# Optimization experiments

Measured on AMD Instinct MI355X. Metric: run time of the kernel, lower is better.

Reference implementation:

```python
import jax, jax.numpy as jnp
import numpy as np

EMBED_DIM = 1024
NUM_HEADS = 16
HEAD_DIM = EMBED_DIM // NUM_HEADS
KERNEL = 3
PAD = KERNEL // 2
B, L = 4, 1024


def conv1d(x, w, b):
    # x: [B, D, L], w: [D_out, D_in, K], b: [D_out]; 'same' padding like nn.Conv1d(padding=K//2)
    y = jax.lax.conv_general_dilated(
        x, w, window_strides=(1,), padding=[(PAD, PAD)],
        dimension_numbers=('NCH', 'OIH', 'NCH'))
    return y + b[None, :, None]


def setup_inputs() -> dict:
    key = jax.random.key(0)
    ks = jax.random.split(key, 12)
    fan = EMBED_DIM * KERNEL
    bound = 1.0 / np.sqrt(fan)
    def wconv(k):
        return jax.random.uniform(k, (EMBED_DIM, EMBED_DIM, KERNEL), jnp.float32, -bound, bound)
    def bconv(k):
        return jax.random.uniform(k, (EMBED_DIM,), jnp.float32, -bound, bound)
    return {
        'query': jax.random.normal(ks[0], (B, L, EMBED_DIM), jnp.float32),
        'key': jax.random.normal(ks[1], (B, L, EMBED_DIM), jnp.float32),
        'value': jax.random.normal(ks[2], (B, L, EMBED_DIM), jnp.float32),
        'key_padding_mask': jax.random.randint(ks[3], (B, L), 0, 2) > 0,
        'attn_mask': jnp.zeros((L, L), jnp.float32),
        'q_w': wconv(ks[4]), 'q_b': bconv(ks[5]),
        'k_w': wconv(ks[6]), 'k_b': bconv(ks[7]),
        'v_w': wconv(ks[8]), 'v_b': bconv(ks[9]),
        'o_w': wconv(ks[10]), 'o_b': bconv(ks[11]),
    }


def reference(query, key, value, key_padding_mask, attn_mask,
              q_w, q_b, k_w, k_b, v_w, v_b, o_w, o_b):
    scale = HEAD_DIM ** -0.5
    # projections: [B, D, L]
    q = conv1d(jnp.swapaxes(query, 1, 2), q_w, q_b)
    k = conv1d(jnp.swapaxes(key, 1, 2), k_w, k_b)
    v = conv1d(jnp.swapaxes(value, 1, 2), v_w, v_b)
    # [B, H, d, L]
    q = q.reshape(B, NUM_HEADS, HEAD_DIM, L)
    k = k.reshape(B, NUM_HEADS, HEAD_DIM, L)
    v = v.reshape(B, NUM_HEADS, HEAD_DIM, L)
    # scores: [B, H, L, L]
    scores = jnp.einsum('bhdi,bhdj->bhij', q, k) * scale
    scores = scores + attn_mask[None, None, :, :]
    scores = jnp.where(key_padding_mask[:, None, None, :], -jnp.inf, scores)
    attn = jax.nn.softmax(scores, axis=-1)  # dropout p=0 (eval) -> identity
    out = jnp.einsum('bhij,bhdj->bhdi', attn, v)  # [B, H, d, L]
    out = out.reshape(B, EMBED_DIM, L)
    out = conv1d(out, o_w, o_b)
    return jnp.swapaxes(out, 1, 2)  # [B, L, D]
```

## Files before the change

kernel.cpp:

```cpp
#include <hip/hip_runtime.h>
#include <math.h>

#define NB 4
#define NL 1024
#define ND 1024
#define NH 16
#define HD 64

typedef __attribute__((ext_vector_type(8))) short bf16x8;
typedef __attribute__((ext_vector_type(4))) float f32x4;

static __device__ __forceinline__ unsigned short f32_to_bf16(float f) {
  unsigned u = __float_as_uint(f);
  u += 0x7FFFu + ((u >> 16) & 1u);
  return (unsigned short)(u >> 16);
}
static __device__ __forceinline__ float bf16_to_f32(unsigned short s) {
  return __uint_as_float(((unsigned)s) << 16);
}

static __device__ __forceinline__ void split8(float4 a, float4 b, bf16x8* hi, bf16x8* lo) {
  unsigned u[8] = {__float_as_uint(a.x), __float_as_uint(a.y),
                   __float_as_uint(a.z), __float_as_uint(a.w),
                   __float_as_uint(b.x), __float_as_uint(b.y),
                   __float_as_uint(b.z), __float_as_uint(b.w)};
  union { unsigned p[4]; bf16x8 v; } H, L;
#pragma unroll
  for (int p = 0; p < 4; ++p) {
    unsigned u0 = u[2 * p], u1 = u[2 * p + 1];
    H.p[p] = __builtin_amdgcn_perm(u1, u0, 0x07060302u);
    unsigned l0 = __float_as_uint(__uint_as_float(u0) - __uint_as_float(u0 & 0xFFFF0000u));
    unsigned l1 = __float_as_uint(__uint_as_float(u1) - __uint_as_float(u1 & 0xFFFF0000u));
    L.p[p] = __builtin_amdgcn_perm(l1, l0, 0x07060302u);
  }
  *hi = H.v; *lo = L.v;
}

__global__ __launch_bounds__(256) void wcvt_kernel(
    const float* __restrict__ w0, const float* __restrict__ w1,
    const float* __restrict__ w2, const float* __restrict__ w3,
    unsigned short* __restrict__ wb, int* __restrict__ flag)
{
  if (blockIdx.x == 0 && blockIdx.y == 0 && threadIdx.x == 0) flag[0] = 0;
  const int t = blockIdx.y;
  const int o = blockIdx.x;
  const float* w = (t == 0) ? w0 : (t == 1) ? w1 : (t == 2) ? w2 : w3;
  unsigned short* hi = wb + (size_t)t * 6 * (1u << 20);
  unsigned short* lo = hi + 3 * (1u << 20);
  const int tid = threadIdx.x;
  float v[12];
  const float* src = w + (size_t)o * (ND * 3) + tid * 12;
#pragma unroll
  for (int j = 0; j < 3; ++j) {
    float4 f = *(const float4*)(src + j * 4);
    v[j * 4 + 0] = f.x; v[j * 4 + 1] = f.y; v[j * 4 + 2] = f.z; v[j * 4 + 3] = f.w;
  }
#pragma unroll
  for (int k = 0; k < 3; ++k) {
    unsigned short hh[4], ll[4];
#pragma unroll
    for (int ii = 0; ii < 4; ++ii) {
      float x = v[ii * 3 + k];
      unsigned short h = f32_to_bf16(x);
      float r = x - bf16_to_f32(h);
      hh[ii] = h; ll[ii] = f32_to_bf16(r);
    }
    size_t dst = (size_t)k * (ND * ND) + (size_t)o * ND + tid * 4;
    *(ushort4*)&hi[dst] = make_ushort4(hh[0], hh[1], hh[2], hh[3]);
    *(ushort4*)&lo[dst] = make_ushort4(ll[0], ll[1], ll[2], ll[3]);
  }
}

__global__ __launch_bounds__(256) void amask_scan(
    const float* __restrict__ a, int* __restrict__ flag)
{
  size_t i = ((size_t)blockIdx.x * 256 + threadIdx.x) * 4;
  float4 v = *(const float4*)&a[i];
  if (v.x != 0.f || v.y != 0.f || v.z != 0.f || v.w != 0.f) atomicOr(flag, 1);
}

__global__ __launch_bounds__(256, 3) void conv_mfma2(
    const float* X0, const float* X1, const float* X2,
    const unsigned short* __restrict__ wb,
    const float* b0, const float* b1, const float* b2,
    float* Y0, float* Y1, float* Y2, int mode)
{
  __shared__ float Af[128 * 32];
  __shared__ unsigned short Bh[128 * 32];
  __shared__ unsigned short Bl[128 * 32];

  const int tid = threadIdx.x, lane = tid & 63, wave = tid >> 6;
  const int lin = blockIdx.x + 8 * (blockIdx.y + 32 * blockIdx.z);
  const int g = lin & 7, t = lin >> 3;
  const int nb = (g & 3) * 2 + (t & 1);
  const int mb = (g >> 2) * 16 + ((t >> 1) & 15);
  const int z  = t >> 5;
  const int n0 = nb * 128, m0 = mb * 128;
  const int b = m0 >> 10, l0v = m0 & (NL - 1);

  const float* X = (mode == 0) ? (z == 0 ? X0 : (z == 1 ? X1 : X2)) : X0;
  const unsigned short* Wh = (mode == 0) ? wb + (size_t)z * 6 * (1u << 20) : wb;
  const unsigned short* Wl = Wh + 3 * (1u << 20);

  const int wm = (wave >> 1) * 64, wn = (wave & 1) * 64;
  const int mrow = lane & 15, quad = lane >> 4;
  const int r16 = lane >> 2, cs = lane & 3;
  const int src_chunk = (cs - (r16 >> 1)) & 3;
  const int bswz = ((quad + (mrow >> 1)) & 3) * 8;

  f32x4 acc[4][4] = {};

  const int kbeg = (mode == 0) ? 0 : z;
  const int kend = (mode == 0) ? 3 : z + 1;
  for (int koff = kbeg; koff < kend; ++koff) {
    const bool edge_lo = (l0v == 0 && koff == 0);
    const bool edge_hi = (l0v == NL - 128 && koff == 2);
    for (int i0 = 0; i0 < ND; i0 += 32) {
#pragma unroll
      for (int s = 0; s < 2; ++s) {
        const int seg = wave * 2 + s;
        const size_t goff = ((size_t)koff << 20) +
                            (size_t)(n0 + seg * 16 + r16) * ND + i0 + src_chunk * 8;
        __builtin_amdgcn_global_load_lds(
            (const __attribute__((address_space(1))) unsigned int*)(Wh + goff),
            (__attribute__((address_space(3))) unsigned int*)&Bh[seg * 512], 16, 0, 0);
        __builtin_amdgcn_global_load_lds(
            (const __attribute__((address_space(1))) unsigned int*)(Wl + goff),
            (__attribute__((address_space(3))) unsigned int*)&Bl[seg * 512], 16, 0, 0);
      }
#pragma unroll
      for (int j = 0; j < 4; ++j) {
        const int s = (wave * 4 + j) * 64 + lane;
        const int row = s >> 3, sir = s & 7;
        const int chunk = (sir - (row & 7)) & 7;
        int l = l0v + row + koff - 1;
        l = (l < 0) ? 0 : (l > NL - 1 ? NL - 1 : l);
        const float* gp = X + ((size_t)(b << 10) + l) * ND + i0 + chunk * 4;
        __builtin_amdgcn_global_load_lds(
            (const __attribute__((address_space(1))) unsigned int*)gp,
            (__attribute__((address_space(3))) unsigned int*)&Af[(wave * 4 + j) * 256],
            16, 0, 0);
      }
      __syncthreads();
      if (edge_lo || edge_hi) {
        const int er = edge_lo ? 0 : 127;
        if (tid < 8) *(float4*)&Af[er * 32 + tid * 4] = make_float4(0.f, 0.f, 0.f, 0.f);
        __syncthreads();
      }
      bf16x8 ah[4], al[4];
#pragma unroll
      for (int mi = 0; mi < 4; ++mi) {
        const int row = wm + mi * 16 + mrow, r7 = row & 7;
        float4 fa = *(const float4*)&Af[row * 32 + (((quad * 2) + r7) & 7) * 4];
        float4 fb = *(const float4*)&Af[row * 32 + (((quad * 2 + 1) + r7) & 7) * 4];
        split8(fa, fb, &ah[mi], &al[mi]);
      }
#pragma unroll
      for (int ni = 0; ni < 4; ++ni) {
        const int brow = wn + ni * 16 + mrow;
        bf16x8 bh = *(const bf16x8*)&Bh[brow * 32 + bswz];
        bf16x8 bl = *(const bf16x8*)&Bl[brow * 32 + bswz];
#pragma unroll
        for (int mi = 0; mi < 4; ++mi) {
          acc[mi][ni] = __builtin_amdgcn_mfma_f32_16x16x32_bf16(ah[mi], bh, acc[mi][ni], 0, 0, 0);
          acc[mi][ni] = __builtin_amdgcn_mfma_f32_16x16x32_bf16(ah[mi], bl, acc[mi][ni], 0, 0, 0);
          acc[mi][ni] = __builtin_amdgcn_mfma_f32_16x16x32_bf16(al[mi], bh, acc[mi][ni], 0, 0, 0);
        }
      }
      __syncthreads();
    }
  }

  if (mode == 0) {
    float* Y = (z == 0) ? Y0 : (z == 1 ? Y1 : Y2);
    const float* bias = (z == 0) ? b0 : (z == 1 ? b1 : b2);
#pragma unroll
    for (int ni = 0; ni < 4; ++ni) {
      const int n = n0 + wn + ni * 16 + mrow;
      const float bv = bias[n];
      const int h = n >> 6, dd = n & 63;
#pragma unroll
      for (int mi = 0; mi < 4; ++mi) {
        const int mbase = m0 + wm + mi * 16 + quad * 4;
        f32x4 v = acc[mi][ni];
#pragma unroll
        for (int r = 0; r < 4; ++r) {
          const int l = (mbase + r) & (NL - 1);
          Y[(((size_t)b * NH + h) * NL + l) * HD + dd] = v[r] + bv;
        }
      }
    }
  } else {
    float* P = Y0 + (size_t)z * ((size_t)NB * NL * ND);
#pragma unroll
    for (int ni = 0; ni < 4; ++ni) {
      const int n = n0 + wn + ni * 16 + mrow;
#pragma unroll
      for (int mi = 0; mi < 4; ++mi) {
        const int mbase = m0 + wm + mi * 16 + quad * 4;
        f32x4 v = acc[mi][ni];
#pragma unroll
        for (int r = 0; r < 4; ++r) {
          const int l = (mbase + r) & (NL - 1);
          P[((size_t)(b << 10) + l) * ND + n] = v[r];
        }
      }
    }
  }
}

__global__ __launch_bounds__(256) void reduce_kernel(
    const float* __restrict__ P, const float* __restrict__ bias, float* __restrict__ out)
{
  const size_t S = (size_t)NB * NL * ND;
  const size_t idx = ((size_t)blockIdx.x * 256 + threadIdx.x) * 4;
  const int n = (int)(idx & (ND - 1));
  float4 p0 = *(const float4*)&P[idx];
  float4 p1 = *(const float4*)&P[idx + S];
  float4 p2 = *(const float4*)&P[idx + 2 * S];
  float4 bv = *(const float4*)&bias[n];
  float4 r;
  r.x = p0.x + p1.x + p2.x + bv.x;
  r.y = p0.y + p1.y + p2.y + bv.y;
  r.z = p0.z + p1.z + p2.z + bv.z;
  r.w = p0.w + p1.w + p2.w + bv.w;
  *(float4*)&out[idx] = r;
}

__global__ __launch_bounds__(256, 3) void attn_mfma(
    const float* __restrict__ qT, const float* __restrict__ kT,
    const float* __restrict__ vT, const int* __restrict__ kpm,
    const float* __restrict__ amask, const int* __restrict__ aflagp,
    float* __restrict__ AO)
{
  __shared__ __align__(16) unsigned short S[3 * 64 * 72];
  unsigned short* Kh = S;
  unsigned short* Kl = S + 4608;
  unsigned short* Vt = S + 2 * 4608;

  const int tid = threadIdx.x, lane = tid & 63, wave = tid >> 6;
  const int c = lane & 15, quad = lane >> 4;
  const int lin = blockIdx.x;
  const int bh = (lin & 7) + 8 * (lin >> 7);
  const int mt = (lin >> 3) & 15;
  const int b = bh >> 4;
  const int m0 = mt * 64;
  const size_t base = (size_t)bh * NL * HD;
  const int aflag = *aflagp;
  const int mrow = wave * 16 + c;
  const int gm = m0 + mrow;

  const int sr = tid >> 2, scq = tid & 3;

#pragma unroll
  for (int ii = 0; ii < 2; ++ii) {
    const int c8 = scq * 2 + ii;
    const float* gp = &qT[base + (size_t)(m0 + sr) * HD + c8 * 8];
    float4 a = *(const float4*)gp, bb = *(const float4*)(gp + 4);
    a.x *= 0.125f; a.y *= 0.125f; a.z *= 0.125f; a.w *= 0.125f;
    bb.x *= 0.125f; bb.y *= 0.125f; bb.z *= 0.125f; bb.w *= 0.125f;
    bf16x8 hi, lo; split8(a, bb, &hi, &lo);
    const int cso = ((c8 + sr) & 7) * 8;
    *(bf16x8*)&Kh[sr * 72 + cso] = hi;
    *(bf16x8*)&Kl[sr * 72 + cso] = lo;
  }
  __syncthreads();
  bf16x8 qbh[2], qbl[2];
#pragma unroll
  for (int kb = 0; kb < 2; ++kb) {
    const int cso = ((kb * 4 + quad + mrow) & 7) * 8;
    qbh[kb] = *(const bf16x8*)&Kh[mrow * 72 + cso];
    qbl[kb] = *(const bf16x8*)&Kl[mrow * 72 + cso];
  }

  f32x4 acc[4] = {};
  float m_r = -INFINITY, l_r = 0.0f;

  for (int n0t = 0; n0t < NL; n0t += 64) {
    __syncthreads();

    float mval[4][4];
#pragma unroll
    for (int nf = 0; nf < 4; ++nf)
#pragma unroll
      for (int r = 0; r < 4; ++r) {
        const int gn = n0t + nf * 16 + quad * 4 + r;
        const bool pm = kpm[b * NL + gn] != 0;
        float am = 0.f;
        if (aflag) am = amask[(size_t)gm * NL + gn];
        mval[nf][r] = pm ? -INFINITY : am;
      }

#pragma unroll
    for (int ii = 0; ii < 2; ++ii) {
      const int c8 = scq * 2 + ii;
      const float* gp = &kT[base + (size_t)(n0t + sr) * HD + c8 * 8];
      float4 a = *(const float4*)gp, bb = *(const float4*)(gp + 4);
      bf16x8 hi, lo; split8(a, bb, &hi, &lo);
      const int cso = ((c8 + sr) & 7) * 8;
      *(bf16x8*)&Kh[sr * 72 + cso] = hi;
      *(bf16x8*)&Kl[sr * 72 + cso] = lo;

      const float* gv = &vT[base + (size_t)(n0t + sr) * HD + c8 * 8];
      float4 va = *(const float4*)gv, vb = *(const float4*)(gv + 4);
      float ve[8] = {va.x, va.y, va.z, va.w, vb.x, vb.y, vb.z, vb.w};
#pragma unroll
      for (int e = 0; e < 8; ++e) {
        const int dd = c8 * 8 + e;
        Vt[dd * 72 + (((sr >> 3) + dd) & 7) * 8 + (sr & 7)] = f32_to_bf16(ve[e]);
      }
    }
    __syncthreads();

    f32x4 sa[4] = {};
#pragma unroll
    for (int kb = 0; kb < 2; ++kb)
#pragma unroll
      for (int nf = 0; nf < 4; ++nf) {
        const int row = nf * 16 + c;
        const int cso = ((kb * 4 + quad + row) & 7) * 8;
        bf16x8 kah = *(const bf16x8*)&Kh[row * 72 + cso];
        bf16x8 kal = *(const bf16x8*)&Kl[row * 72 + cso];
        sa[nf] = __builtin_amdgcn_mfma_f32_16x16x32_bf16(kah, qbh[kb], sa[nf], 0, 0, 0);
        sa[nf] = __builtin_amdgcn_mfma_f32_16x16x32_bf16(kah, qbl[kb], sa[nf], 0, 0, 0);
        sa[nf] = __builtin_amdgcn_mfma_f32_16x16x32_bf16(kal, qbh[kb], sa[nf], 0, 0, 0);
      }

    float p[4][4];
    float tmax = -INFINITY;
#pragma unroll
    for (int nf = 0; nf < 4; ++nf)
#pragma unroll
      for (int r = 0; r < 4; ++r) {
        float s = sa[nf][r] + mval[nf][r];
        p[nf][r] = s;
        tmax = fmaxf(tmax, s);
      }
    tmax = fmaxf(tmax, __shfl_xor(tmax, 16));
    tmax = fmaxf(tmax, __shfl_xor(tmax, 32));
    const float newm = fmaxf(m_r, tmax);
    const float msafe = (newm == -INFINITY) ? 0.f : newm;
    const float alpha = __expf(m_r - msafe);
    float rs = 0.f;
#pragma unroll
    for (int nf = 0; nf < 4; ++nf)
#pragma unroll
      for (int r = 0; r < 4; ++r) {
        float e = __expf(p[nf][r] - msafe);
        p[nf][r] = e;
        rs += e;
      }
    rs += __shfl_xor(rs, 16);
    rs += __shfl_xor(rs, 32);
    l_r = l_r * alpha + rs;
    m_r = newm;
#pragma unroll
    for (int df = 0; df < 4; ++df) {
      acc[df][0] *= alpha; acc[df][1] *= alpha;
      acc[df][2] *= alpha; acc[df][3] *= alpha;
    }

    unsigned q16[4][2];
#pragma unroll
    for (int nf = 0; nf < 4; ++nf)
#pragma unroll
      for (int w = 0; w < 2; ++w)
        q16[nf][w] = (unsigned)f32_to_bf16(p[nf][2 * w]) |
                     ((unsigned)f32_to_bf16(p[nf][2 * w + 1]) << 16);

#pragma unroll
    for (int kb = 0; kb < 2; ++kb) {
      union { unsigned d[4]; bf16x8 v; } pb;
#pragma unroll
      for (int w = 0; w < 4; ++w) {
        const int addr = ((((quad & 1) * 2 + (w >> 1)) * 16 + c) << 2);
        unsigned v0 = __builtin_amdgcn_ds_bpermute(addr, (int)q16[2 * kb][w & 1]);
        unsigned v1 = __builtin_amdgcn_ds_bpermute(addr, (int)q16[2 * kb + 1][w & 1]);
        pb.d[w] = (quad >> 1) ? v1 : v0;
      }
#pragma unroll
      for (int df = 0; df < 4; ++df) {
        const int row = df * 16 + c;
        const int cso = ((kb * 4 + quad + row) & 7) * 8;
        bf16x8 va = *(const bf16x8*)&Vt[row * 72 + cso];
        acc[df] = __builtin_amdgcn_mfma_f32_16x16x32_bf16(va, pb.v, acc[df], 0, 0, 0);
      }
    }
  }

  __syncthreads();
  const float inv = 1.0f / l_r;
  float* Ob = (float*)S + wave * (16 * 68);
#pragma unroll
  for (int df = 0; df < 4; ++df)
#pragma unroll
    for (int r = 0; r < 4; ++r)
      Ob[c * 68 + df * 16 + quad * 4 + r] = acc[df][r] * inv;
  __syncthreads();
  const int mr2 = lane >> 2, cq2 = lane & 3;
  const int h = bh & 15;
#pragma unroll
  for (int ii = 0; ii < 4; ++ii) {
    const int chunk = cq2 * 4 + ii;
    float4 v = *(const float4*)&Ob[mr2 * 68 + chunk * 4];
    *(float4*)&AO[((size_t)(b << 10) + (m0 + wave * 16 + mr2)) * ND +
                  h * HD + chunk * 4] = v;
  }
}

extern "C" void kernel_launch(void* const* d_in, const int* in_sizes, int n_in,
                              void* d_out, int out_size, void* d_ws, size_t ws_size,
                              hipStream_t stream) {
  (void)in_sizes; (void)n_in; (void)out_size; (void)ws_size;
  const float* query = (const float*)d_in[0];
  const float* key_  = (const float*)d_in[1];
  const float* value = (const float*)d_in[2];
  const int*   kpm   = (const int*)d_in[3];
  const float* amask = (const float*)d_in[4];
  const float* q_w = (const float*)d_in[5];
  const float* q_b = (const float*)d_in[6];
  const float* k_w = (const float*)d_in[7];
  const float* k_b = (const float*)d_in[8];
  const float* v_w = (const float*)d_in[9];
  const float* v_b = (const float*)d_in[10];
  const float* o_w = (const float*)d_in[11];
  const float* o_b = (const float*)d_in[12];
  float* out = (float*)d_out;

  unsigned short* Wb = (unsigned short*)d_ws;
  float* qT = (float*)((char*)d_ws + (size_t)50331648);
  float* kT = qT + (size_t)NB * NL * ND;
  float* vT = kT + (size_t)NB * NL * ND;
  float* P  = qT;
  float* AO = (float*)d_ws;
  int* flag = (int*)d_out;

  wcvt_kernel<<<dim3(1024, 4), 256, 0, stream>>>(q_w, k_w, v_w, o_w, Wb, flag);
  amask_scan<<<1024, 256, 0, stream>>>(amask, flag);
  conv_mfma2<<<dim3(8, 32, 3), 256, 0, stream>>>(
      query, key_, value, Wb, q_b, k_b, v_b, qT, kT, vT, 0);
  attn_mfma<<<1024, 256, 0, stream>>>(qT, kT, vT, kpm, amask, flag, AO);
  conv_mfma2<<<dim3(8, 32, 3), 256, 0, stream>>>(
      AO, AO, AO, Wb + (size_t)3 * 6 * (1u << 20), o_b, o_b, o_b, P, P, P, 1);
  reduce_kernel<<<4096, 256, 0, stream>>>(P, o_b, out);
}
```

Measured before the change: 514.4 us.

## Pre-split Q/K into bf16 hi/lo planes and stream tiles via global_load_lds

The QKV projection epilogue now writes Q (pre-scaled by scale*log2e) and K as bf16 hi/lo planes and V as transposed bf16, so the attention kernel no longer converts fp32 per tile. The attention kernel fills LDS directly with global_load_lds, caches the key padding mask in LDS, switches to exp2, skips rescaling when the running max grows by at most 8, and raises wave priority around the MFMA blocks. This reduces global read traffic and per-tile ALU work in attention. In exchange the projection epilogue does scattered 2-byte stores, and the rescale skip relies on fp32 headroom.

Result: faster. 499.8 us (-2.8%).

```diff
diff --git a/kernel.cpp b/kernel.cpp
--- a/kernel.cpp
+++ b/kernel.cpp
@@ -17,6 +17,11 @@
 }
 static __device__ __forceinline__ float bf16_to_f32(unsigned short s) {
   return __uint_as_float(((unsigned)s) << 16);
+}
+static __device__ __forceinline__ float exp2_f(float x) {
+  float r;
+  asm("v_exp_f32 %0, %1" : "=v"(r) : "v"(x));
+  return r;
 }
 
 static __device__ __forceinline__ void split8(float4 a, float4 b, bf16x8* hi, bf16x8* lo) {
@@ -172,21 +177,52 @@
   }
 
   if (mode == 0) {
-    float* Y = (z == 0) ? Y0 : (z == 1 ? Y1 : Y2);
     const float* bias = (z == 0) ? b0 : (z == 1 ? b1 : b2);
-#pragma unroll
-    for (int ni = 0; ni < 4; ++ni) {
-      const int n = n0 + wn + ni * 16 + mrow;
-      const float bv = bias[n];
-      const int h = n >> 6, dd = n & 63;
-#pragma unroll
-      for (int mi = 0; mi < 4; ++mi) {
-        const int mbase = m0 + wm + mi * 16 + quad * 4;
-        f32x4 v = acc[mi][ni];
-#pragma unroll
-        for (int r = 0; r < 4; ++r) {
-          const int l = (mbase + r) & (NL - 1);
-          Y[(((size_t)b * NH + h) * NL + l) * HD + dd] = v[r] + bv;
+    unsigned short* U = (unsigned short*)Y0;
+    const size_t PLs = (size_t)NB * NL * ND / NH * NH;
+    if (z < 2) {
+      unsigned short* Ph = U + (size_t)(2 * z) * PLs;
+      unsigned short* Pl = Ph + PLs;
+      const float sc = (z == 0) ? 0.18033688011112042f : 1.0f;
+#pragma unroll
+      for (int ni = 0; ni < 4; ++ni) {
+        const int n = n0 + wn + ni * 16 + mrow;
+        const float bv = bias[n];
+        const int h = n >> 6, dd = n & 63;
+        const int bh = b * NH + h;
+#pragma unroll
+        for (int mi = 0; mi < 4; ++mi) {
+          const int mbase = m0 + wm + mi * 16 + quad * 4;
+          f32x4 v = acc[mi][ni];
+#pragma unroll
+          for (int r = 0; r < 4; ++r) {
+            const int l = (mbase + r) & (NL - 1);
+            const float val = (v[r] + bv) * sc;
+            const unsigned u = __float_as_uint(val);
+            const unsigned short hh = (unsigned short)(u >> 16);
+            const float res = val - __uint_as_float(u & 0xFFFF0000u);
+            const unsigned short ll = (unsigned short)(__float_as_uint(res) >> 16);
+            const size_t off = ((size_t)bh * NL + l) * HD + dd;
+            Ph[off] = hh; Pl[off] = ll;
+          }
+        }
+      }
+    } else {
+      unsigned short* Pv = U + (size_t)4 * PLs;
+#pragma unroll
+      for (int ni = 0; ni < 4; ++ni) {
+        const int n = n0 + wn + ni * 16 + mrow;
+        const float bv = bias[n];
+        const int h = n >> 6, dd = n & 63;
+        const int bh = b * NH + h;
+#pragma unroll
+        for (int mi = 0; mi < 4; ++mi) {
+          const int mbase = m0 + wm + mi * 16 + quad * 4;
+          const int lb = mbase & (NL - 1);
+          f32x4 v = acc[mi][ni];
+          ushort4 s4 = make_ushort4(f32_to_bf16(v[0] + bv), f32_to_bf16(v[1] + bv),
+                                    f32_to_bf16(v[2] + bv), f32_to_bf16(v[3] + bv));
+          *(ushort4*)&Pv[((size_t)bh * HD + dd) * NL + lb] = s4;
         }
       }
     }
@@ -228,15 +264,15 @@
 }
 
 __global__ __launch_bounds__(256, 3) void attn_mfma(
-    const float* __restrict__ qT, const float* __restrict__ kT,
-    const float* __restrict__ vT, const int* __restrict__ kpm,
+    const unsigned short* __restrict__ U, const int* __restrict__ kpm,
     const float* __restrict__ amask, const int* __restrict__ aflagp,
     float* __restrict__ AO)
 {
-  __shared__ __align__(16) unsigned short S[3 * 64 * 72];
+  __shared__ __align__(16) unsigned short S[3 * 4096];
+  __shared__ __align__(16) float Fm[NL];
   unsigned short* Kh = S;
-  unsigned short* Kl = S + 4608;
-  unsigned short* Vt = S + 2 * 4608;
+  unsigned short* Kl = S + 4096;
+  unsigned short* Vt = S + 8192;
 
   const int tid = threadIdx.x, lane = tid & 63, wave = tid >> 6;
   const int c = lane & 15, quad = lane >> 4;
@@ -245,32 +281,49 @@
   const int mt = (lin >> 3) & 15;
   const int b = bh >> 4;
   const int m0 = mt * 64;
-  const size_t base = (size_t)bh * NL * HD;
   const int aflag = *aflagp;
   const int mrow = wave * 16 + c;
   const int gm = m0 + mrow;
 
-  const int sr = tid >> 2, scq = tid & 3;
-
-#pragma unroll
-  for (int ii = 0; ii < 2; ++ii) {
-    const int c8 = scq * 2 + ii;
-    const float* gp = &qT[base + (size_t)(m0 + sr) * HD + c8 * 8];
-    float4 a = *(const float4*)gp, bb = *(const float4*)(gp + 4);
-    a.x *= 0.125f; a.y *= 0.125f; a.z *= 0.125f; a.w *= 0.125f;
-    bb.x *= 0.125f; bb.y *= 0.125f; bb.z *= 0.125f; bb.w *= 0.125f;
-    bf16x8 hi, lo; split8(a, bb, &hi, &lo);
-    const int cso = ((c8 + sr) & 7) * 8;
-    *(bf16x8*)&Kh[sr * 72 + cso] = hi;
-    *(bf16x8*)&Kl[sr * 72 + cso] = lo;
+  const size_t PLs = (size_t)4096 * 1024;
+  const unsigned short* qTh = U;
+  const unsigned short* qTl = U + PLs;
+  const unsigned short* kTh = U + 2 * PLs;
+  const unsigned short* kTl = U + 3 * PLs;
+  const unsigned short* vTt = U + 4 * PLs;
+
+  const int srow = lane >> 3;
+  const int slot = lane & 7;
+  const int chunk = (slot - srow) & 7;
+
+#pragma unroll
+  for (int q = 0; q < 4; ++q) {
+    const int pl = q >> 1;
+    const int i = wave * 2 + (q & 1);
+    const int row = i * 8 + srow;
+    const unsigned short* src = (pl ? qTl : qTh) +
+        ((size_t)bh * NL + m0 + row) * HD + chunk * 8;
+    unsigned short* dst = (pl ? Kl : Kh) + i * 512;
+    __builtin_amdgcn_global_load_lds(
+        (const __attribute__((address_space(1))) unsigned int*)src,
+        (__attribute__((address_space(3))) unsigned int*)dst, 16, 0, 0);
+  }
+  {
+    int4 kv = *(const int4*)&kpm[b * NL + tid * 4];
+    float4 f;
+    f.x = kv.x ? -INFINITY : 0.f;
+    f.y = kv.y ? -INFINITY : 0.f;
+    f.z = kv.z ? -INFINITY : 0.f;
+    f.w = kv.w ? -INFINITY : 0.f;
+    *(float4*)&Fm[tid * 4] = f;
   }
   __syncthreads();
   bf16x8 qbh[2], qbl[2];
 #pragma unroll
   for (int kb = 0; kb < 2; ++kb) {
     const int cso = ((kb * 4 + quad + mrow) & 7) * 8;
-    qbh[kb] = *(const bf16x8*)&Kh[mrow * 72 + cso];
-    qbl[kb] = *(const bf16x8*)&Kl[mrow * 72 + cso];
+    qbh[kb] = *(const bf16x8*)&Kh[mrow * 64 + cso];
+    qbl[kb] = *(const bf16x8*)&Kl[mrow * 64 + cso];
   }
 
   f32x4 acc[4] = {};
@@ -279,52 +332,53 @@
   for (int n0t = 0; n0t < NL; n0t += 64) {
     __syncthreads();
 
+#pragma unroll
+    for (int q = 0; q < 6; ++q) {
+      const int pl = q >> 1;
+      const int i = wave * 2 + (q & 1);
+      const int row = i * 8 + srow;
+      const unsigned short* src;
+      unsigned short* dst;
+      if (pl == 0)      { src = kTh + ((size_t)bh * NL + n0t + row) * HD + chunk * 8; dst = Kh + i * 512; }
+      else if (pl == 1) { src = kTl + ((size_t)bh * NL + n0t + row) * HD + chunk * 8; dst = Kl + i * 512; }
+      else              { src = vTt + ((size_t)bh * HD + row) * NL + n0t + chunk * 8; dst = Vt + i * 512; }
+      __builtin_amdgcn_global_load_lds(
+          (const __attribute__((address_space(1))) unsigned int*)src,
+          (__attribute__((address_space(3))) unsigned int*)dst, 16, 0, 0);
+    }
+
     float mval[4][4];
 #pragma unroll
-    for (int nf = 0; nf < 4; ++nf)
-#pragma unroll
-      for (int r = 0; r < 4; ++r) {
-        const int gn = n0t + nf * 16 + quad * 4 + r;
-        const bool pm = kpm[b * NL + gn] != 0;
-        float am = 0.f;
-        if (aflag) am = amask[(size_t)gm * NL + gn];
-        mval[nf][r] = pm ? -INFINITY : am;
-      }
-
-#pragma unroll
-    for (int ii = 0; ii < 2; ++ii) {
-      const int c8 = scq * 2 + ii;
-      const float* gp = &kT[base + (size_t)(n0t + sr) * HD + c8 * 8];
-      float4 a = *(const float4*)gp, bb = *(const float4*)(gp + 4);
-      bf16x8 hi, lo; split8(a, bb, &hi, &lo);
-      const int cso = ((c8 + sr) & 7) * 8;
-      *(bf16x8*)&Kh[sr * 72 + cso] = hi;
-      *(bf16x8*)&Kl[sr * 72 + cso] = lo;
-
-      const float* gv = &vT[base + (size_t)(n0t + sr) * HD + c8 * 8];
-      float4 va = *(const float4*)gv, vb = *(const float4*)(gv + 4);
-      float ve[8] = {va.x, va.y, va.z, va.w, vb.x, vb.y, vb.z, vb.w};
-#pragma unroll
-      for (int e = 0; e < 8; ++e) {
-        const int dd = c8 * 8 + e;
-        Vt[dd * 72 + (((sr >> 3) + dd) & 7) * 8 + (sr & 7)] = f32_to_bf16(ve[e]);
-      }
+    for (int nf = 0; nf < 4; ++nf) {
+      float4 fm = *(const float4*)&Fm[n0t + nf * 16 + quad * 4];
+      mval[nf][0] = fm.x; mval[nf][1] = fm.y; mval[nf][2] = fm.z; mval[nf][3] = fm.w;
+    }
+    if (aflag) {
+#pragma unroll
+      for (int nf = 0; nf < 4; ++nf)
+#pragma unroll
+        for (int r = 0; r < 4; ++r) {
+          const int gn = n0t + nf * 16 + quad * 4 + r;
+          mval[nf][r] += amask[(size_t)gm * NL + gn] * 1.4426950408889634f;
+        }
     }
     __syncthreads();
 
     f32x4 sa[4] = {};
+    __builtin_amdgcn_s_setprio(1);
 #pragma unroll
     for (int kb = 0; kb < 2; ++kb)
 #pragma unroll
       for (int nf = 0; nf < 4; ++nf) {
         const int row = nf * 16 + c;
         const int cso = ((kb * 4 + quad + row) & 7) * 8;
-        bf16x8 kah = *(const bf16x8*)&Kh[row * 72 + cso];
-        bf16x8 kal = *(const bf16x8*)&Kl[row * 72 + cso];
+        bf16x8 kah = *(const bf16x8*)&Kh[row * 64 + cso];
+        bf16x8 kal = *(const bf16x8*)&Kl[row * 64 + cso];
         sa[nf] = __builtin_amdgcn_mfma_f32_16x16x32_bf16(kah, qbh[kb], sa[nf], 0, 0, 0);
         sa[nf] = __builtin_amdgcn_mfma_f32_16x16x32_bf16(kah, qbl[kb], sa[nf], 0, 0, 0);
         sa[nf] = __builtin_amdgcn_mfma_f32_16x16x32_bf16(kal, qbh[kb], sa[nf], 0, 0, 0);
       }
+    __builtin_amdgcn_s_setprio(0);
 
     float p[4][4];
     float tmax = -INFINITY;
@@ -338,26 +392,41 @@
       }
     tmax = fmaxf(tmax, __shfl_xor(tmax, 16));
     tmax = fmaxf(tmax, __shfl_xor(tmax, 32));
-    const float newm = fmaxf(m_r, tmax);
-    const float msafe = (newm == -INFINITY) ? 0.f : newm;
-    const float alpha = __expf(m_r - msafe);
     float rs = 0.f;
-#pragma unroll
-    for (int nf = 0; nf < 4; ++nf)
-#pragma unroll
-      for (int r = 0; r < 4; ++r) {
-        float e = __expf(p[nf][r] - msafe);
-        p[nf][r] = e;
-        rs += e;
-      }
-    rs += __shfl_xor(rs, 16);
-    rs += __shfl_xor(rs, 32);
-    l_r = l_r * alpha + rs;
-    m_r = newm;
-#pragma unroll
-    for (int df = 0; df < 4; ++df) {
-      acc[df][0] *= alpha; acc[df][1] *= alpha;
-      acc[df][2] *= alpha; acc[df][3] *= alpha;
+    if (__all(tmax - m_r <= 8.0f)) {
+      const float msafe = m_r;
+#pragma unroll
+      for (int nf = 0; nf < 4; ++nf)
+#pragma unroll
+        for (int r = 0; r < 4; ++r) {
+          float e = exp2_f(p[nf][r] - msafe);
+          p[nf][r] = e;
+          rs += e;
+        }
+      rs += __shfl_xor(rs, 16);
+      rs += __shfl_xor(rs, 32);
+      l_r += rs;
+    } else {
+      const float newm = fmaxf(m_r, tmax);
+      const float msafe = (newm == -INFINITY) ? 0.f : newm;
+      const float alpha = exp2_f(m_r - msafe);
+#pragma unroll
+      for (int nf = 0; nf < 4; ++nf)
+#pragma unroll
+        for (int r = 0; r < 4; ++r) {
+          float e = exp2_f(p[nf][r] - msafe);
+          p[nf][r] = e;
+          rs += e;
+        }
+      rs += __shfl_xor(rs, 16);
+      rs += __shfl_xor(rs, 32);
+      l_r = l_r * alpha + rs;
+      m_r = newm;
+#pragma unroll
+      for (int df = 0; df < 4; ++df) {
+        acc[df][0] *= alpha; acc[df][1] *= alpha;
+        acc[df][2] *= alpha; acc[df][3] *= alpha;
+      }
     }
 
     unsigned q16[4][2];
@@ -378,13 +447,15 @@
         unsigned v1 = __builtin_amdgcn_ds_bpermute(addr, (int)q16[2 * kb + 1][w & 1]);
         pb.d[w] = (quad >> 1) ? v1 : v0;
       }
+      __builtin_amdgcn_s_setprio(1);
 #pragma unroll
       for (int df = 0; df < 4; ++df) {
         const int row = df * 16 + c;
         const int cso = ((kb * 4 + quad + row) & 7) * 8;
-        bf16x8 va = *(const bf16x8*)&Vt[row * 72 + cso];
+        bf16x8 va = *(const bf16x8*)&Vt[row * 64 + cso];
         acc[df] = __builtin_amdgcn_mfma_f32_16x16x32_bf16(va, pb.v, acc[df], 0, 0, 0);
       }
+      __builtin_amdgcn_s_setprio(0);
     }
   }
 
@@ -401,10 +472,10 @@
   const int h = bh & 15;
 #pragma unroll
   for (int ii = 0; ii < 4; ++ii) {
-    const int chunk = cq2 * 4 + ii;
-    float4 v = *(const float4*)&Ob[mr2 * 68 + chunk * 4];
+    const int chunk2 = cq2 * 4 + ii;
+    float4 v = *(const float4*)&Ob[mr2 * 68 + chunk2 * 4];
     *(float4*)&AO[((size_t)(b << 10) + (m0 + wave * 16 + mr2)) * ND +
-                  h * HD + chunk * 4] = v;
+                  h * HD + chunk2 * 4] = v;
   }
 }
 
@@ -428,18 +499,16 @@
   float* out = (float*)d_out;
 
   unsigned short* Wb = (unsigned short*)d_ws;
-  float* qT = (float*)((char*)d_ws + (size_t)50331648);
-  float* kT = qT + (size_t)NB * NL * ND;
-  float* vT = kT + (size_t)NB * NL * ND;
-  float* P  = qT;
+  unsigned short* U  = (unsigned short*)((char*)d_ws + (size_t)50331648);
+  float* P  = (float*)((char*)d_ws + (size_t)50331648);
   float* AO = (float*)d_ws;
   int* flag = (int*)d_out;
 
   wcvt_kernel<<<dim3(1024, 4), 256, 0, stream>>>(q_w, k_w, v_w, o_w, Wb, flag);
   amask_scan<<<1024, 256, 0, stream>>>(amask, flag);
   conv_mfma2<<<dim3(8, 32, 3), 256, 0, stream>>>(
-      query, key_, value, Wb, q_b, k_b, v_b, qT, kT, vT, 0);
-  attn_mfma<<<1024, 256, 0, stream>>>(qT, kT, vT, kpm, amask, flag, AO);
+      query, key_, value, Wb, q_b, k_b, v_b, (float*)U, (float*)U, (float*)U, 0);
+  attn_mfma<<<1024, 256, 0, stream>>>(U, kpm, amask, flag, AO);
   conv_mfma2<<<dim3(8, 32, 3), 256, 0, stream>>>(
       AO, AO, AO, Wb + (size_t)3 * 6 * (1u << 20), o_b, o_b, o_b, P, P, P, 1);
   reduce_kernel<<<4096, 256, 0, stream>>>(P, o_b, out);
```
